# Performance work log

Hardware: AMD Instinct MI355X
Metric: run time of the kernel (lower is better)

The kernel has to match this reference:

```python
import jax, jax.numpy as jnp
import numpy as np

H, T, D = 16, 2048, 1024
DH = D // H  # 64


def setup_inputs() -> dict:
    key = jax.random.key(0)
    ks = jax.random.split(key, 6)
    state = jax.random.normal(ks[0], (H, DH, DH), jnp.float32) * 0.02  # per-head recurrent state
    x = jax.random.normal(ks[1], (T, D), jnp.float32)
    done = jax.random.uniform(ks[2], (T,)) < (4.0 / T)  # sparse episode-reset flags (bool)
    w_qkv = jax.random.normal(ks[3], (D, 3 * D), jnp.float32) / np.sqrt(D)
    b_qkv = jnp.zeros((3 * D,), jnp.float32)
    w_out = jax.random.normal(ks[4], (D, D), jnp.float32) / np.sqrt(D)
    b_out = jnp.zeros((D,), jnp.float32)
    return {"state": state, "x": x, "done": done, "w_qkv": w_qkv,
            "b_qkv": b_qkv, "w_out": w_out, "b_out": b_out}


def _mha_forward(state, x, done, w_qkv, b_qkv, w_out, b_out):
    # qkv projection; einops 'T (QKV H Dh) -> QKV H T Dh'
    qkv = (x @ w_qkv + b_qkv).reshape(T, 3, H, DH).transpose(1, 2, 0, 3)
    q, k, v = qkv[0], qkv[1], qkv[2]  # each (H, T, Dh)

    cum = jnp.cumsum(done.astype(jnp.int32))  # inclusive cumsum, as in done.cumsum()
    before_first = cum == 0            # tokens before first reset (attend to carried state)
    after_last = cum == cum[-1]        # tokens after last reset (feed new state)
    done_any = cum[-1] > 0

    # make_attn_mask(done): causal AND no reset index i with s < i <= t.
    # The scanned mask equals: causal & (cum[t] == cum[s]) (same-segment).
    t_idx = jnp.arange(T)
    mask = (t_idx[:, None] >= t_idx[None, :]) & (cum[:, None] == cum[None, :])  # (T, T)

    attn = jnp.where(mask[None], jnp.einsum('htd,hsd->hts', q, k), 0.0)  # mask * (q @ k.T)
    q_bef = q * before_first[None, :, None]
    out = jnp.einsum('hts,hsd->htd', attn, v) + jnp.einsum('htd,hde->hte', q_bef, state)

    k_aft = k * after_last[None, :, None]
    v_aft = v * after_last[None, :, None]
    s_new = jnp.einsum('htd,hte->hde', k_aft, v_aft)  # k_aft.T @ v_aft per head
    new_state = jnp.where(done_any, s_new, state + s_new)

    # 'H T Dh -> T (H Dh)' then output projection
    x_out = out.transpose(1, 0, 2).reshape(T, D) @ w_out + b_out
    return new_state, x_out


def reference(state, x, done, w_qkv, b_qkv, w_out, b_out):
    return _mha_forward(state, x, done, w_qkv, b_qkv, w_out, b_out)
```

## Files before the change

### kernel.cpp

```cpp
#include <hip/hip_runtime.h>

#define TT 2048
#define DD 1024
#define HH 16
#define DH 64
#define QKV_N 3072
#define QKW 2048

typedef __attribute__((ext_vector_type(8))) short bf16x8;
typedef __attribute__((ext_vector_type(4))) short short4v;
typedef __attribute__((ext_vector_type(4))) float f32x4;

__device__ inline short f2bf(float f) {
    union { float f; unsigned u; } v; v.f = f;
    unsigned r = v.u + 0x7fff + ((v.u >> 16) & 1);
    return (short)(r >> 16);
}

__device__ inline f32x4 mfma16(bf16x8 a, bf16x8 b, f32x4 c) {
    return __builtin_amdgcn_mfma_f32_16x16x32_bf16(a, b, c, 0, 0, 0);
}

__device__ __forceinline__ void gload16(const void* g, void* l) {
    __builtin_amdgcn_global_load_lds(
        (const __attribute__((address_space(1))) unsigned int*)g,
        (__attribute__((address_space(3))) unsigned int*)l, 16, 0, 0);
}

__device__ void transpose_tile(const float* __restrict__ in, short* __restrict__ out,
                               int R, int C, int r0, int c0, float (*tile)[65]) {
    int tid = threadIdx.x;
#pragma unroll
    for (int p = 0; p < 4; ++p) {
        int ch = tid + p * 256;
        int r = ch >> 4, c4 = (ch & 15) * 4;
        float4 v = *(const float4*)&in[(size_t)(r0 + r) * C + c0 + c4];
        tile[r][c4] = v.x; tile[r][c4 + 1] = v.y; tile[r][c4 + 2] = v.z; tile[r][c4 + 3] = v.w;
    }
    __syncthreads();
#pragma unroll
    for (int p = 0; p < 2; ++p) {
        int ch = tid + p * 256;
        int c = ch >> 3, r8 = (ch & 7) * 8;
        short tmp[8];
#pragma unroll
        for (int i = 0; i < 8; ++i) tmp[i] = f2bf(tile[r8 + i][c]);
        *(float4*)&out[(size_t)(c0 + c) * R + r0 + r8] = *(float4*)tmp;
    }
}

__global__ __launch_bounds__(256) void prep_kernel(const float* __restrict__ x,
                                                   const float* __restrict__ w_qkv,
                                                   const float* __restrict__ w_out,
                                                   const float* __restrict__ state,
                                                   const int* __restrict__ done,
                                                   short* __restrict__ x_bf,
                                                   short* __restrict__ wqT,
                                                   short* __restrict__ woT,
                                                   short* __restrict__ stT,
                                                   float* __restrict__ stout,
                                                   int* __restrict__ seg,
                                                   int* __restrict__ totalp,
                                                   int* __restrict__ aux) {
    __shared__ float tile[64][65];
    __shared__ int scanbuf[2048 + 512 + 1];
    int b = blockIdx.x;
    int tid = threadIdx.x;
    if (b < 1024) {
        int i = (b * 256 + tid) * 8;
        float4 a = *(const float4*)&x[i];
        float4 c = *(const float4*)&x[i + 4];
        short tmp[8] = {f2bf(a.x), f2bf(a.y), f2bf(a.z), f2bf(a.w),
                        f2bf(c.x), f2bf(c.y), f2bf(c.z), f2bf(c.w)};
        *(float4*)&x_bf[i] = *(float4*)tmp;
    } else if (b < 1792) {
        int bb = b - 1024;
        transpose_tile(w_qkv, wqT, DD, QKV_N, (bb & 15) * 64, (bb >> 4) * 64, tile);
    } else if (b < 2048) {
        int bb = b - 1792;
        transpose_tile(w_out, woT, DD, DD, (bb & 15) * 64, (bb >> 4) * 64, tile);
    } else if (b < 2064) {
        int h = b - 2048;
        transpose_tile(state + (size_t)h * 4096, stT + (size_t)h * 4096, DH, DH, 0, 0, tile);
    } else if (b < 2128) {
        __shared__ int anyf;
        if (tid == 0) anyf = 0;
        __syncthreads();
        int acc = 0;
#pragma unroll
        for (int i = 0; i < 8; ++i) acc |= done[tid * 8 + i];
        if (acc) anyf = 1;
        __syncthreads();
        int f = ((b - 2064) * 256 + tid) * 4;
        float4 v = anyf ? make_float4(0.f, 0.f, 0.f, 0.f) : *(const float4*)&state[f];
        *(float4*)&stout[f] = v;
    } else {
        int* segl = scanbuf;
        int* part = scanbuf + 2048;
        int* excl = scanbuf + 2304;
        int base = tid * 8;
        int local[8];
        int run = 0;
#pragma unroll
        for (int i = 0; i < 8; ++i) { run += (done[base + i] != 0) ? 1 : 0; local[i] = run; }
        part[tid] = run;
        __syncthreads();
        if (tid < 64) {
            int p4[4];
#pragma unroll
            for (int i = 0; i < 4; ++i) p4[i] = part[tid * 4 + i];
            int s = p4[0] + p4[1] + p4[2] + p4[3];
            int v = s;
#pragma unroll
            for (int off = 1; off < 64; off <<= 1) {
                int u = __shfl_up(v, off);
                if (tid >= off) v += u;
            }
            int ex = v - s;
#pragma unroll
            for (int i = 0; i < 4; ++i) { excl[tid * 4 + i] = ex; ex += p4[i]; }
            if (tid == 63) { totalp[0] = v; scanbuf[2560] = v; }
        }
        __syncthreads();
        int off = excl[tid];
#pragma unroll
        for (int i = 0; i < 8; ++i) {
            int sv = off + local[i];
            seg[base + i] = sv;
            segl[base + i] = sv;
        }
        __syncthreads();
        if (tid < 33) {
            int target = (tid < 32) ? segl[tid * 64] : scanbuf[2560];
            int lo = 0, hi = 2047;
            while (lo < hi) { int mid = (lo + hi) >> 1; if (segl[mid] >= target) hi = mid; else lo = mid + 1; }
            aux[tid] = lo >> 6;
        }
    }
}

__global__ __launch_bounds__(256, 3) void gemm_qkv(const short* __restrict__ A,
                                                   const short* __restrict__ BT,
                                                   const float* __restrict__ bias,
                                                   short* __restrict__ qk,
                                                   short* __restrict__ vt) {
    __shared__ __align__(16) short As[2][2][64 * 32];
    __shared__ __align__(16) short Bs[2][2][128 * 32];
    const int K = DD;
    int tid = threadIdx.x;
    int wave = tid >> 6, lane = tid & 63;
    int quad = lane >> 4, l15 = lane & 15;
    int m0 = blockIdx.x * 64, n0 = blockIdx.y * 128;
    int wr = (wave >> 1) * 32, wc = (wave & 1) * 64;

    int srow = wave * 16 + (lane >> 2);
    int scol = (lane & 3) * 8;
    const short* Ag = A + (size_t)(m0 + srow) * K + scol;
    const short* Bg = BT + (size_t)(n0 + srow) * K + scol;

#pragma unroll
    for (int ks = 0; ks < 2; ++ks) {
        gload16(Ag + ks * 32, &As[0][ks][(wave * 16) * 32]);
        gload16(Bg + ks * 32, &Bs[0][ks][(wave * 16) * 32]);
        gload16(Bg + (size_t)64 * K + ks * 32, &Bs[0][ks][(64 + wave * 16) * 32]);
    }
    __syncthreads();

    f32x4 acc[2][4] = {};
    int cur = 0;
    for (int k0 = 0; k0 < K; k0 += 64, cur ^= 1) {
        if (k0 + 64 < K) {
#pragma unroll
            for (int ks = 0; ks < 2; ++ks) {
                gload16(Ag + k0 + 64 + ks * 32, &As[cur ^ 1][ks][(wave * 16) * 32]);
                gload16(Bg + k0 + 64 + ks * 32, &Bs[cur ^ 1][ks][(wave * 16) * 32]);
                gload16(Bg + (size_t)64 * K + k0 + 64 + ks * 32,
                        &Bs[cur ^ 1][ks][(64 + wave * 16) * 32]);
            }
        }
#pragma unroll
        for (int ks = 0; ks < 2; ++ks) {
            bf16x8 af[2], bfr[4];
#pragma unroll
            for (int i = 0; i < 2; ++i)
                af[i]  = *(const bf16x8*)&As[cur][ks][(wr + i * 16 + l15) * 32 + quad * 8];
#pragma unroll
            for (int j = 0; j < 4; ++j)
                bfr[j] = *(const bf16x8*)&Bs[cur][ks][(wc + j * 16 + l15) * 32 + quad * 8];
#pragma unroll
            for (int i = 0; i < 2; ++i)
#pragma unroll
                for (int j = 0; j < 4; ++j)
                    acc[i][j] = mfma16(af[i], bfr[j], acc[i][j]);
        }
        __syncthreads();
    }

    if (n0 < 2048) {
#pragma unroll
        for (int i = 0; i < 2; ++i)
#pragma unroll
            for (int j = 0; j < 4; ++j)
#pragma unroll
                for (int r = 0; r < 4; ++r) {
                    int row = m0 + wr + i * 16 + quad * 4 + r;
                    int col = n0 + wc + j * 16 + l15;
                    qk[(size_t)row * QKW + col] = f2bf(acc[i][j][r] + bias[col]);
                }
    } else {
#pragma unroll
        for (int j = 0; j < 4; ++j) {
            int col = n0 + wc + j * 16 + l15;
            float bv = bias[col];
            int eg = col - 2048;
            int hh = eg >> 6, e = eg & 63;
#pragma unroll
            for (int i = 0; i < 2; ++i) {
                int tb = m0 + wr + i * 16 + quad * 4;
                short4v pk;
#pragma unroll
                for (int r = 0; r < 4; ++r) pk[r] = f2bf(acc[i][j][r] + bv);
                *(short4v*)&vt[(size_t)hh * (DH * TT) + (size_t)e * TT + tb] = pk;
            }
        }
    }
}

__global__ __launch_bounds__(256) void attn_mfma(const short* __restrict__ qk,
                                                 const short* __restrict__ vt,
                                                 const short* __restrict__ stT,
                                                 const int* __restrict__ seg,
                                                 const int* __restrict__ totalp,
                                                 const int* __restrict__ aux,
                                                 short* __restrict__ outb,
                                                 float* __restrict__ nsout) {
    __shared__ __align__(16) short Qh[2][64 * 32];
    __shared__ __align__(16) short Kh[2][2][64 * 32];
    __shared__ __align__(16) short Vh[2][2][64 * 32];
    __shared__ __align__(16) short Ss[64 * 72];

    int h = blockIdx.x, tt = blockIdx.y, z = blockIdx.z;
    int t0 = tt * 64;
    int tid = threadIdx.x, wave = tid >> 6, lane = tid & 63;
    int quad = lane >> 4, l15 = lane & 15;
    int myt = wave * 16;
    const short* vbase = vt + (size_t)h * (DH * TT);

    if (z == 1) {
        if (tt < aux[32]) return;
        int total = totalp[0];
        int myd = wave * 16;
        short* K0 = Kh[0][0];
        short* K1 = Kh[0][1];
        bool keep = (seg[t0 + lane] == total);
        const short* src = qk + (size_t)(t0 + lane) * QKW + 1024 + h * DH + myd;
        union { float4 f; short s[8]; } u0, u1;
        u0.f = keep ? *(const float4*)src : make_float4(0.f, 0.f, 0.f, 0.f);
        u1.f = keep ? *(const float4*)(src + 8) : make_float4(0.f, 0.f, 0.f, 0.f);
        short* dst = (lane < 32) ? &K0[lane] : &K1[lane - 32];
#pragma unroll
        for (int i = 0; i < 8; ++i) {
            dst[(myd + i) * 32] = u0.s[i];
            dst[(myd + 8 + i) * 32] = u1.s[i];
        }
        bf16x8 a0 = *(const bf16x8*)&K0[(myd + l15) * 32 + quad * 8];
        bf16x8 a1 = *(const bf16x8*)&K1[(myd + l15) * 32 + quad * 8];
        f32x4 acc2[4] = {};
#pragma unroll
        for (int j = 0; j < 4; ++j) {
            const short* vrow = vbase + (size_t)(j * 16 + l15) * TT + t0 + quad * 8;
            bf16x8 b0 = *(const bf16x8*)vrow;
            bf16x8 b1 = *(const bf16x8*)(vrow + 32);
            acc2[j] = mfma16(a0, b0, acc2[j]);
            acc2[j] = mfma16(a1, b1, acc2[j]);
        }
        float* oh = nsout + (size_t)h * 4096;
#pragma unroll
        for (int j = 0; j < 4; ++j)
#pragma unroll
            for (int r = 0; r < 4; ++r)
                atomicAdd(&oh[(myd + quad * 4 + r) * DH + j * 16 + l15], acc2[j][r]);
        return;
    }

    int st0 = aux[tt];
    int sr = lane >> 2;
    int ch = lane & 3;
    const short* kg = qk + 1024 + h * DH;

    {
#pragma unroll
        for (int h2 = 0; h2 < 2; ++h2)
            gload16(qk + (size_t)(t0 + myt + sr) * QKW + h * DH + h2 * 32 + ch * 8,
                    &Qh[h2][myt * 32]);
        int s0 = st0 * 64;
        gload16(kg + (size_t)(s0 + myt + sr) * QKW + ch * 8,      &Kh[0][0][myt * 32]);
        gload16(kg + (size_t)(s0 + myt + sr) * QKW + 32 + ch * 8, &Kh[0][1][myt * 32]);
        gload16(vbase + (size_t)(myt + sr) * TT + s0 + ch * 8,    &Vh[0][0][myt * 32]);
        gload16(vbase + (size_t)(myt + sr) * TT + s0 + 32 + ch * 8, &Vh[0][1][myt * 32]);
    }
    __syncthreads();

    bf16x8 af[2];
#pragma unroll
    for (int h2 = 0; h2 < 2; ++h2)
        af[h2] = *(const bf16x8*)&Qh[h2][(myt + l15) * 32 + quad * 8];

    int t_val = t0 + myt + l15;
    int seg_lane = seg[t_val];

    f32x4 acc2[4] = {};
    if (seg[t0] == 0) {
        const short* sb = stT + (size_t)h * 4096;
#pragma unroll
        for (int j = 0; j < 4; ++j)
#pragma unroll
            for (int h2 = 0; h2 < 2; ++h2) {
                bf16x8 a = *(const bf16x8*)(sb + (j * 16 + l15) * 64 + h2 * 32 + quad * 8);
                acc2[j] = mfma16(a, af[h2], acc2[j]);
            }
        if (seg_lane != 0) {
#pragma unroll
            for (int j = 0; j < 4; ++j)
#pragma unroll
                for (int r = 0; r < 4; ++r) acc2[j][r] = 0.f;
        }
    }

    int p = 0;
    for (int st = st0; st <= tt; ++st, p ^= 1) {
        if (st != st0) __syncthreads();
        if (st + 1 <= tt) {
            int s1 = (st + 1) * 64;
            gload16(kg + (size_t)(s1 + myt + sr) * QKW + ch * 8,        &Kh[p ^ 1][0][myt * 32]);
            gload16(kg + (size_t)(s1 + myt + sr) * QKW + 32 + ch * 8,   &Kh[p ^ 1][1][myt * 32]);
            gload16(vbase + (size_t)(myt + sr) * TT + s1 + ch * 8,      &Vh[p ^ 1][0][myt * 32]);
            gload16(vbase + (size_t)(myt + sr) * TT + s1 + 32 + ch * 8, &Vh[p ^ 1][1][myt * 32]);
        }
        int s0 = st * 64;

        f32x4 sacc[4] = {};
#pragma unroll
        for (int j = 0; j < 4; ++j)
#pragma unroll
            for (int h2 = 0; h2 < 2; ++h2) {
                bf16x8 kb = *(const bf16x8*)&Kh[p][h2][(j * 16 + l15) * 32 + quad * 8];
                sacc[j] = mfma16(kb, af[h2], sacc[j]);
            }
        int4 seg4[4];
#pragma unroll
        for (int j = 0; j < 4; ++j)
            seg4[j] = *(const int4*)&seg[s0 + j * 16 + quad * 4];
#pragma unroll
        for (int j = 0; j < 4; ++j) {
            short4v pk;
#pragma unroll
            for (int r = 0; r < 4; ++r) {
                int s_val = s0 + j * 16 + quad * 4 + r;
                int sv = (r == 0) ? seg4[j].x : (r == 1) ? seg4[j].y : (r == 2) ? seg4[j].z : seg4[j].w;
                bool ok = (sv == seg_lane) && (s_val <= t_val);
                pk[r] = ok ? f2bf(sacc[j][r]) : (short)0;
            }
            *(short4v*)&Ss[(myt + l15) * 72 + j * 16 + quad * 4] = pk;
        }
        bf16x8 sf[2];
#pragma unroll
        for (int h2 = 0; h2 < 2; ++h2)
            sf[h2] = *(const bf16x8*)&Ss[(myt + l15) * 72 + h2 * 32 + quad * 8];
#pragma unroll
        for (int j = 0; j < 4; ++j)
#pragma unroll
            for (int h2 = 0; h2 < 2; ++h2) {
                bf16x8 vb = *(const bf16x8*)&Vh[p][h2][(j * 16 + l15) * 32 + quad * 8];
                acc2[j] = mfma16(vb, sf[h2], acc2[j]);
            }
    }

#pragma unroll
    for (int j = 0; j < 4; ++j) {
        short4v pk;
#pragma unroll
        for (int r = 0; r < 4; ++r) pk[r] = f2bf(acc2[j][r]);
        *(short4v*)&outb[(size_t)t_val * DD + h * DH + j * 16 + quad * 4] = pk;
    }
}

__global__ __launch_bounds__(256) void gemm_out(const short* __restrict__ A,
                                                const short* __restrict__ BT,
                                                const float* __restrict__ bias,
                                                float* __restrict__ x_out) {
    __shared__ __align__(16) short As[2][2][64 * 32];
    __shared__ __align__(16) short Bs[2][2][128 * 32];
    const int K = DD, N = DD;
    int tid = threadIdx.x;
    int wave = tid >> 6, lane = tid & 63;
    int quad = lane >> 4, l15 = lane & 15;
    int m0 = blockIdx.x * 64, n0 = blockIdx.y * 128;
    int wr = (wave >> 1) * 32, wc = (wave & 1) * 64;

    int srow = wave * 16 + (lane >> 2);
    int scol = (lane & 3) * 8;
    const short* Ag = A + (size_t)(m0 + srow) * K + scol;
    const short* Bg = BT + (size_t)(n0 + srow) * K + scol;

#pragma unroll
    for (int ks = 0; ks < 2; ++ks) {
        gload16(Ag + ks * 32, &As[0][ks][(wave * 16) * 32]);
        gload16(Bg + ks * 32, &Bs[0][ks][(wave * 16) * 32]);
        gload16(Bg + (size_t)64 * K + ks * 32, &Bs[0][ks][(64 + wave * 16) * 32]);
    }
    __syncthreads();

    f32x4 acc[2][4] = {};
    int cur = 0;
    for (int k0 = 0; k0 < K; k0 += 64, cur ^= 1) {
        if (k0 + 64 < K) {
#pragma unroll
            for (int ks = 0; ks < 2; ++ks) {
                gload16(Ag + k0 + 64 + ks * 32, &As[cur ^ 1][ks][(wave * 16) * 32]);
                gload16(Bg + k0 + 64 + ks * 32, &Bs[cur ^ 1][ks][(wave * 16) * 32]);
                gload16(Bg + (size_t)64 * K + k0 + 64 + ks * 32,
                        &Bs[cur ^ 1][ks][(64 + wave * 16) * 32]);
            }
        }
#pragma unroll
        for (int ks = 0; ks < 2; ++ks) {
            bf16x8 af[2], bfr[4];
#pragma unroll
            for (int i = 0; i < 2; ++i)
                af[i]  = *(const bf16x8*)&As[cur][ks][(wr + i * 16 + l15) * 32 + quad * 8];
#pragma unroll
            for (int j = 0; j < 4; ++j)
                bfr[j] = *(const bf16x8*)&Bs[cur][ks][(wc + j * 16 + l15) * 32 + quad * 8];
#pragma unroll
            for (int i = 0; i < 2; ++i)
#pragma unroll
                for (int j = 0; j < 4; ++j)
                    acc[i][j] = mfma16(af[i], bfr[j], acc[i][j]);
        }
        __syncthreads();
    }

#pragma unroll
    for (int i = 0; i < 2; ++i)
#pragma unroll
        for (int j = 0; j < 4; ++j) {
            int col = n0 + wc + j * 16 + l15;
            float bv = bias[col];
#pragma unroll
            for (int r = 0; r < 4; ++r) {
                int row = m0 + wr + i * 16 + quad * 4 + r;
                x_out[(size_t)row * N + col] = acc[i][j][r] + bv;
            }
        }
}

extern "C" void kernel_launch(void* const* d_in, const int* in_sizes, int n_in,
                              void* d_out, int out_size, void* d_ws, size_t ws_size,
                              hipStream_t stream) {
    const float* state = (const float*)d_in[0];
    const float* x     = (const float*)d_in[1];
    const int*   done  = (const int*)d_in[2];
    const float* w_qkv = (const float*)d_in[3];
    const float* b_qkv = (const float*)d_in[4];
    const float* w_out = (const float*)d_in[5];
    const float* b_out = (const float*)d_in[6];

    char* ws = (char*)d_ws;
    int*   seg    = (int*)ws;
    int*   totalp = (int*)(ws + 8192);
    int*   aux    = (int*)(ws + 8256);
    short* wqT    = (short*)(ws + 8448);
    short* woT    = (short*)(ws + 6299904);
    short* stT    = (short*)(ws + 8397056);
    short* qk     = (short*)(ws + 8528128);
    short* vt     = (short*)(ws + 16916736);
    short* xbf_outb = (short*)(ws + 21111040);

    float* new_state_out = (float*)d_out;
    float* x_out         = (float*)d_out + HH * DH * DH;

    prep_kernel<<<2129, 256, 0, stream>>>(x, w_qkv, w_out, state, done,
                                          xbf_outb, wqT, woT, stT,
                                          new_state_out, seg, totalp, aux);

    gemm_qkv<<<dim3(TT / 64, QKV_N / 128), 256, 0, stream>>>(
        xbf_outb, wqT, b_qkv, qk, vt);

    attn_mfma<<<dim3(HH, TT / 64, 2), 256, 0, stream>>>(
        qk, vt, stT, seg, totalp, aux, xbf_outb, new_state_out);

    gemm_out<<<dim3(TT / 64, DD / 128), 256, 0, stream>>>(
        xbf_outb, woT, b_out, x_out);
}
```

Baseline: 147.2 us.

## Triple-buffer LDS in QKV and output GEMMs with single barrier per tile

```diff
diff --git a/kernel.cpp b/kernel.cpp
--- a/kernel.cpp
+++ b/kernel.cpp
@@ -139,14 +139,15 @@
     }
 }
 
-__global__ __launch_bounds__(256, 3) void gemm_qkv(const short* __restrict__ A,
+__global__ __launch_bounds__(256, 2) void gemm_qkv(const short* __restrict__ A,
                                                    const short* __restrict__ BT,
                                                    const float* __restrict__ bias,
                                                    short* __restrict__ qk,
                                                    short* __restrict__ vt) {
-    __shared__ __align__(16) short As[2][2][64 * 32];
-    __shared__ __align__(16) short Bs[2][2][128 * 32];
+    __shared__ __align__(16) short As[3][2][64 * 32];
+    __shared__ __align__(16) short Bs[3][2][128 * 32];
     const int K = DD;
+    const int NT = 16;
     int tid = threadIdx.x;
     int wave = tid >> 6, lane = tid & 63;
     int quad = lane >> 4, l15 = lane & 15;
@@ -158,43 +159,54 @@
     const short* Ag = A + (size_t)(m0 + srow) * K + scol;
     const short* Bg = BT + (size_t)(n0 + srow) * K + scol;
 
-#pragma unroll
-    for (int ks = 0; ks < 2; ++ks) {
-        gload16(Ag + ks * 32, &As[0][ks][(wave * 16) * 32]);
-        gload16(Bg + ks * 32, &Bs[0][ks][(wave * 16) * 32]);
-        gload16(Bg + (size_t)64 * K + ks * 32, &Bs[0][ks][(64 + wave * 16) * 32]);
-    }
-    __syncthreads();
+#define STAGE_QKV(t, buf)                                                     \
+    {                                                                         \
+        int k0 = (t) * 64;                                                    \
+        _Pragma("unroll")                                                     \
+        for (int ks = 0; ks < 2; ++ks) {                                      \
+            gload16(Ag + k0 + ks * 32, &As[buf][ks][(wave * 16) * 32]);       \
+            gload16(Bg + k0 + ks * 32, &Bs[buf][ks][(wave * 16) * 32]);       \
+            gload16(Bg + (size_t)64 * K + k0 + ks * 32,                       \
+                    &Bs[buf][ks][(64 + wave * 16) * 32]);                     \
+        }                                                                     \
+    }
+
+    STAGE_QKV(0, 0);
+    STAGE_QKV(1, 1);
 
     f32x4 acc[2][4] = {};
-    int cur = 0;
-    for (int k0 = 0; k0 < K; k0 += 64, cur ^= 1) {
-        if (k0 + 64 < K) {
-#pragma unroll
-            for (int ks = 0; ks < 2; ++ks) {
-                gload16(Ag + k0 + 64 + ks * 32, &As[cur ^ 1][ks][(wave * 16) * 32]);
-                gload16(Bg + k0 + 64 + ks * 32, &Bs[cur ^ 1][ks][(wave * 16) * 32]);
-                gload16(Bg + (size_t)64 * K + k0 + 64 + ks * 32,
-                        &Bs[cur ^ 1][ks][(64 + wave * 16) * 32]);
-            }
+    int rd = 0, st = 2;
+#pragma unroll 1
+    for (int t = 0; t < NT; ++t) {
+        if (t < NT - 1) {
+            asm volatile("s_waitcnt vmcnt(6)" ::: "memory");
+        } else {
+            asm volatile("s_waitcnt vmcnt(0)" ::: "memory");
+        }
+        __builtin_amdgcn_s_barrier();
+        __builtin_amdgcn_sched_barrier(0);
+        if (t + 2 < NT) {
+            STAGE_QKV(t + 2, st);
+            st = (st + 1 == 3) ? 0 : st + 1;
         }
 #pragma unroll
         for (int ks = 0; ks < 2; ++ks) {
             bf16x8 af[2], bfr[4];
 #pragma unroll
             for (int i = 0; i < 2; ++i)
-                af[i]  = *(const bf16x8*)&As[cur][ks][(wr + i * 16 + l15) * 32 + quad * 8];
+                af[i]  = *(const bf16x8*)&As[rd][ks][(wr + i * 16 + l15) * 32 + quad * 8];
 #pragma unroll
             for (int j = 0; j < 4; ++j)
-                bfr[j] = *(const bf16x8*)&Bs[cur][ks][(wc + j * 16 + l15) * 32 + quad * 8];
+                bfr[j] = *(const bf16x8*)&Bs[rd][ks][(wc + j * 16 + l15) * 32 + quad * 8];
 #pragma unroll
             for (int i = 0; i < 2; ++i)
 #pragma unroll
                 for (int j = 0; j < 4; ++j)
                     acc[i][j] = mfma16(af[i], bfr[j], acc[i][j]);
         }
-        __syncthreads();
-    }
+        rd = (rd + 1 == 3) ? 0 : rd + 1;
+    }
+#undef STAGE_QKV
 
     if (n0 < 2048) {
 #pragma unroll
@@ -385,13 +397,14 @@
     }
 }
 
-__global__ __launch_bounds__(256) void gemm_out(const short* __restrict__ A,
-                                                const short* __restrict__ BT,
-                                                const float* __restrict__ bias,
-                                                float* __restrict__ x_out) {
-    __shared__ __align__(16) short As[2][2][64 * 32];
-    __shared__ __align__(16) short Bs[2][2][128 * 32];
+__global__ __launch_bounds__(256, 2) void gemm_out(const short* __restrict__ A,
+                                                   const short* __restrict__ BT,
+                                                   const float* __restrict__ bias,
+                                                   float* __restrict__ x_out) {
+    __shared__ __align__(16) short As[3][2][64 * 32];
+    __shared__ __align__(16) short Bs[3][2][128 * 32];
     const int K = DD, N = DD;
+    const int NT = 16;
     int tid = threadIdx.x;
     int wave = tid >> 6, lane = tid & 63;
     int quad = lane >> 4, l15 = lane & 15;
@@ -403,43 +416,54 @@
     const short* Ag = A + (size_t)(m0 + srow) * K + scol;
     const short* Bg = BT + (size_t)(n0 + srow) * K + scol;
 
-#pragma unroll
-    for (int ks = 0; ks < 2; ++ks) {
-        gload16(Ag + ks * 32, &As[0][ks][(wave * 16) * 32]);
-        gload16(Bg + ks * 32, &Bs[0][ks][(wave * 16) * 32]);
-        gload16(Bg + (size_t)64 * K + ks * 32, &Bs[0][ks][(64 + wave * 16) * 32]);
-    }
-    __syncthreads();
+#define STAGE_OUT(t, buf)                                                     \
+    {                                                                         \
+        int k0 = (t) * 64;                                                    \
+        _Pragma("unroll")                                                     \
+        for (int ks = 0; ks < 2; ++ks) {                                      \
+            gload16(Ag + k0 + ks * 32, &As[buf][ks][(wave * 16) * 32]);       \
+            gload16(Bg + k0 + ks * 32, &Bs[buf][ks][(wave * 16) * 32]);       \
+            gload16(Bg + (size_t)64 * K + k0 + ks * 32,                       \
+                    &Bs[buf][ks][(64 + wave * 16) * 32]);                     \
+        }                                                                     \
+    }
+
+    STAGE_OUT(0, 0);
+    STAGE_OUT(1, 1);
 
     f32x4 acc[2][4] = {};
-    int cur = 0;
-    for (int k0 = 0; k0 < K; k0 += 64, cur ^= 1) {
-        if (k0 + 64 < K) {
-#pragma unroll
-            for (int ks = 0; ks < 2; ++ks) {
-                gload16(Ag + k0 + 64 + ks * 32, &As[cur ^ 1][ks][(wave * 16) * 32]);
-                gload16(Bg + k0 + 64 + ks * 32, &Bs[cur ^ 1][ks][(wave * 16) * 32]);
-                gload16(Bg + (size_t)64 * K + k0 + 64 + ks * 32,
-                        &Bs[cur ^ 1][ks][(64 + wave * 16) * 32]);
-            }
+    int rd = 0, st = 2;
+#pragma unroll 1
+    for (int t = 0; t < NT; ++t) {
+        if (t < NT - 1) {
+            asm volatile("s_waitcnt vmcnt(6)" ::: "memory");
+        } else {
+            asm volatile("s_waitcnt vmcnt(0)" ::: "memory");
+        }
+        __builtin_amdgcn_s_barrier();
+        __builtin_amdgcn_sched_barrier(0);
+        if (t + 2 < NT) {
+            STAGE_OUT(t + 2, st);
+            st = (st + 1 == 3) ? 0 : st + 1;
         }
 #pragma unroll
         for (int ks = 0; ks < 2; ++ks) {
             bf16x8 af[2], bfr[4];
 #pragma unroll
             for (int i = 0; i < 2; ++i)
-                af[i]  = *(const bf16x8*)&As[cur][ks][(wr + i * 16 + l15) * 32 + quad * 8];
+                af[i]  = *(const bf16x8*)&As[rd][ks][(wr + i * 16 + l15) * 32 + quad * 8];
 #pragma unroll
             for (int j = 0; j < 4; ++j)
-                bfr[j] = *(const bf16x8*)&Bs[cur][ks][(wc + j * 16 + l15) * 32 + quad * 8];
+                bfr[j] = *(const bf16x8*)&Bs[rd][ks][(wc + j * 16 + l15) * 32 + quad * 8];
 #pragma unroll
             for (int i = 0; i < 2; ++i)
 #pragma unroll
                 for (int j = 0; j < 4; ++j)
                     acc[i][j] = mfma16(af[i], bfr[j], acc[i][j]);
         }
-        __syncthreads();
-    }
+        rd = (rd + 1 == 3) ? 0 : rd + 1;
+    }
+#undef STAGE_OUT
 
 #pragma unroll
     for (int i = 0; i < 2; ++i)
```

Result: slower. 152.7 us (+3.7%).
